# Kernel tuning notes

Measured on AMD Instinct MI355X. Metric: run time of the kernel, lower is better.

Reference implementation:

```python
import math
import jax, jax.numpy as jnp
from jax import lax
import numpy as np

L, B, S, H, N = 2, 1, 2048, 1024, 16
HN = H // N
EPS = 1e-5
SIGMA = 0.02
OUT_STD = SIGMA / math.sqrt(2.0 * L)


def gelu(x):
    # OpenAI tanh-approx gelu, matching gelu_impl
    return 0.5 * x * (1.0 + jnp.tanh(0.7978845608028654 * x * (1.0 + 0.044715 * x * x)))


def layer_norm(x, g, b):
    mu = jnp.mean(x, axis=-1, keepdims=True)
    var = jnp.mean(jnp.square(x - mu), axis=-1, keepdims=True)
    return (x - mu) / jnp.sqrt(var + EPS) * g + b


def setup_inputs() -> dict:
    key = jax.random.key(0)
    ks = jax.random.split(key, 8)
    x = jax.random.normal(ks[0], (B, S, H), dtype=jnp.float32)
    ltor_mask = jnp.tril(jnp.ones((S, S), dtype=jnp.float32))[None, None]  # [1,1,S,S]
    return {
        "hidden_states": x,
        "ltor_mask": ltor_mask,
        "ln1_g": jnp.ones((L, H), jnp.float32),
        "ln1_b": jnp.zeros((L, H), jnp.float32),
        "qkv_w": jax.random.normal(ks[1], (L, H, 3 * H), jnp.float32) * SIGMA,
        "qkv_b": jnp.zeros((L, 3 * H), jnp.float32),
        "dense_w": jax.random.normal(ks[2], (L, H, H), jnp.float32) * OUT_STD,
        "dense_b": jnp.zeros((L, H), jnp.float32),
        "ln2_g": jnp.ones((L, H), jnp.float32),
        "ln2_b": jnp.zeros((L, H), jnp.float32),
        "fc_w": jax.random.normal(ks[3], (L, H, 4 * H), jnp.float32) * SIGMA,
        "fc_b": jnp.zeros((L, 4 * H), jnp.float32),
        "proj_w": jax.random.normal(ks[4], (L, 4 * H, H), jnp.float32) * OUT_STD,
        "proj_b": jnp.zeros((L, H), jnp.float32),
        "lnf_g": jnp.ones((H,), jnp.float32),
        "lnf_b": jnp.zeros((H,), jnp.float32),
    }


def _transformer(hidden_states, ltor_mask, ln1_g, ln1_b, qkv_w, qkv_b, dense_w, dense_b,
                 ln2_g, ln2_b, fc_w, fc_b, proj_w, proj_b, lnf_g, lnf_b):
    scale = 1.0 / math.sqrt(HN)

    def step(h, p):
        g1, b1, qw, qb, dw, db, g2, b2, fw, fb, pw, pb = p
        y = layer_norm(h, g1, b1)
        qkv = y @ qw + qb                       # [B,S,3H]
        q, k, v = jnp.split(qkv, 3, axis=-1)
        # [B,S,H] -> [B,N,S,HN]
        q = q.reshape(B, S, N, HN).transpose(0, 2, 1, 3)
        k = k.reshape(B, S, N, HN).transpose(0, 2, 1, 3)
        v = v.reshape(B, S, N, HN).transpose(0, 2, 1, 3)
        scores = jnp.einsum('bnqd,bnkd->bnqk', q, k) * scale
        scores = scores * ltor_mask - 10000.0 * (1.0 - ltor_mask)
        probs = jax.nn.softmax(scores, axis=-1)
        ctx = jnp.einsum('bnqk,bnkd->bnqd', probs, v)
        ctx = ctx.transpose(0, 2, 1, 3).reshape(B, S, H)
        attn_out = ctx @ dw + db
        h2 = h + attn_out
        y2 = layer_norm(h2, g2, b2)
        mlp_out = gelu(y2 @ fw + fb) @ pw + pb
        return h2 + mlp_out, None

    params = (ln1_g, ln1_b, qkv_w, qkv_b, dense_w, dense_b,
              ln2_g, ln2_b, fc_w, fc_b, proj_w, proj_b)
    h, _ = lax.scan(step, hidden_states, params)
    return layer_norm(h, lnf_g, lnf_b)


def reference(hidden_states, ltor_mask, ln1_g, ln1_b, qkv_w, qkv_b, dense_w, dense_b,
              ln2_g, ln2_b, fc_w, fc_b, proj_w, proj_b, lnf_g, lnf_b):
    return _transformer(hidden_states, ltor_mask, ln1_g, ln1_b, qkv_w, qkv_b,
                        dense_w, dense_b, ln2_g, ln2_b, fc_w, fc_b,
                        proj_w, proj_b, lnf_g, lnf_b)
```

## Files before the change

kernel.cpp:

```cpp
#include <hip/hip_runtime.h>
#include <hip/hip_bf16.h>
#include <cstdint>
#include <cstddef>

typedef __bf16 bf16;
typedef __attribute__((ext_vector_type(4))) __bf16 bf16x4;
typedef __attribute__((ext_vector_type(8))) __bf16 bf16x8;
typedef __attribute__((ext_vector_type(4))) float floatx4;

__global__ __launch_bounds__(256) void ln_first(const float* __restrict__ x,
                                                float* __restrict__ h,
                                                const float* __restrict__ g,
                                                const float* __restrict__ b,
                                                bf16* __restrict__ y) {
    __shared__ float red[8];
    const int row = blockIdx.x, tid = threadIdx.x;
    const size_t off = (size_t)row * 1024 + tid * 4;
    const float4 v = *(const float4*)(x + off);
    *(float4*)(h + off) = v;
    float s = v.x + v.y + v.z + v.w;
#pragma unroll
    for (int o = 32; o > 0; o >>= 1) s += __shfl_xor(s, o);
    if ((tid & 63) == 0) red[tid >> 6] = s;
    __syncthreads();
    const float mean = (red[0] + red[1] + red[2] + red[3]) * (1.f / 1024.f);
    const float d[4] = {v.x - mean, v.y - mean, v.z - mean, v.w - mean};
    float q = d[0] * d[0] + d[1] * d[1] + d[2] * d[2] + d[3] * d[3];
#pragma unroll
    for (int o = 32; o > 0; o >>= 1) q += __shfl_xor(q, o);
    if ((tid & 63) == 0) red[4 + (tid >> 6)] = q;
    __syncthreads();
    const float var = (red[4] + red[5] + red[6] + red[7]) * (1.f / 1024.f);
    const float rstd = rsqrtf(var + 1e-5f);
    const int base = tid * 4;
#pragma unroll
    for (int i = 0; i < 4; i++)
        y[off + i] = (bf16)(d[i] * rstd * g[base + i] + b[base + i]);
}

template <typename OutT, int KS>
__global__ __launch_bounds__(256) void reduce_ln(const bf16* __restrict__ part,
                                                 const float* __restrict__ bias,
                                                 float* __restrict__ h,
                                                 const float* __restrict__ g,
                                                 const float* __restrict__ b,
                                                 OutT* __restrict__ y) {
    __shared__ float red[8];
    const int row = blockIdx.x, tid = threadIdx.x;
    const int base = tid * 4;
    const size_t off = (size_t)row * 1024 + base;
    const float4 hv = *(const float4*)(h + off);
    const float4 bv = *(const float4*)(bias + base);
    float a[4] = {hv.x + bv.x, hv.y + bv.y, hv.z + bv.z, hv.w + bv.w};
#pragma unroll
    for (int z = 0; z < KS; z++) {
        bf16x4 pv = *(const bf16x4*)(part + (size_t)z * (2048 * 1024) + off);
#pragma unroll
        for (int i = 0; i < 4; i++) a[i] += (float)pv[i];
    }
    *(float4*)(h + off) = (float4){a[0], a[1], a[2], a[3]};
    float s = a[0] + a[1] + a[2] + a[3];
#pragma unroll
    for (int o = 32; o > 0; o >>= 1) s += __shfl_xor(s, o);
    if ((tid & 63) == 0) red[tid >> 6] = s;
    __syncthreads();
    const float mean = (red[0] + red[1] + red[2] + red[3]) * (1.f / 1024.f);
    const float d[4] = {a[0] - mean, a[1] - mean, a[2] - mean, a[3] - mean};
    float q = d[0] * d[0] + d[1] * d[1] + d[2] * d[2] + d[3] * d[3];
#pragma unroll
    for (int o = 32; o > 0; o >>= 1) q += __shfl_xor(q, o);
    if ((tid & 63) == 0) red[4 + (tid >> 6)] = q;
    __syncthreads();
    const float var = (red[4] + red[5] + red[6] + red[7]) * (1.f / 1024.f);
    const float rstd = rsqrtf(var + 1e-5f);
#pragma unroll
    for (int i = 0; i < 4; i++)
        y[off + i] = (OutT)(d[i] * rstd * g[base + i] + b[base + i]);
}

__global__ __launch_bounds__(256) void transpose_cvt(const float* __restrict__ in,
                                                     bf16* __restrict__ out, int K, int N) {
    __shared__ float T[64][65];
    const int k0 = blockIdx.x * 64, n0 = blockIdx.y * 64;
    {
        const int r = threadIdx.x >> 4;
        const int c4 = (threadIdx.x & 15) * 4;
#pragma unroll
        for (int j = 0; j < 4; j++) {
            float4 v = *(const float4*)&in[(size_t)(k0 + r + j * 16) * N + n0 + c4];
            T[r + j * 16][c4 + 0] = v.x; T[r + j * 16][c4 + 1] = v.y;
            T[r + j * 16][c4 + 2] = v.z; T[r + j * 16][c4 + 3] = v.w;
        }
    }
    __syncthreads();
    {
        const int rn = threadIdx.x >> 3;
        const int c8 = (threadIdx.x & 7) * 8;
#pragma unroll
        for (int j = 0; j < 2; j++) {
            bf16x8 v;
#pragma unroll
            for (int i = 0; i < 8; i++) v[i] = (bf16)T[c8 + i][rn + j * 32];
            *(bf16x8*)&out[(size_t)(n0 + rn + j * 32) * K + k0 + c8] = v;
        }
    }
}

template <int MODE, int BM>
__global__ __launch_bounds__(256) void gemm_bt(const bf16* __restrict__ A,
                                               const bf16* __restrict__ BT,
                                               const float* __restrict__ bias,
                                               bf16* __restrict__ outb,
                                               int M, int N, int K) {
    constexpr int MS = BM / 32;
    constexpr int AC = BM / 32;
    constexpr int LS = 72;
    __shared__ bf16 As[BM * LS];
    __shared__ bf16 Bs[128 * LS];
    const int tid = threadIdx.x;
    const int w = tid >> 6, lane = tid & 63;
    const int quad = lane >> 4, l16 = lane & 15;
    const int wm = w >> 1, wn = w & 1;
    const int m0 = blockIdx.x * BM, n0 = blockIdx.y * 128;
    const int kchunk = K / gridDim.z;
    const int kbeg = blockIdx.z * kchunk, kend = kbeg + kchunk;

    const int srow = lane >> 3;
    const int scol = (lane & 7) * 8;
    const int arow = w * (BM / 4) + srow;
    const int brow = w * 32 + srow;
    const bf16* ga = A + (size_t)(m0 + arow) * K + scol;
    const bf16* gb = BT + (size_t)(n0 + brow) * K + scol;
    bf16* wa = &As[arow * LS + scol];
    bf16* wb = &Bs[brow * LS + scol];

    bf16x8 areg[AC], breg[4];
#pragma unroll
    for (int s = 0; s < AC; s++) areg[s] = *(const bf16x8*)(ga + (size_t)(s * 8) * K + kbeg);
#pragma unroll
    for (int s = 0; s < 4; s++) breg[s] = *(const bf16x8*)(gb + (size_t)(s * 8) * K + kbeg);

    floatx4 acc[MS][4];
#pragma unroll
    for (int i = 0; i < MS; i++)
#pragma unroll
        for (int j = 0; j < 4; j++) acc[i][j] = (floatx4){0.f, 0.f, 0.f, 0.f};

    for (int k0 = kbeg; k0 < kend; k0 += 64) {
        __syncthreads();
#pragma unroll
        for (int s = 0; s < AC; s++) *(bf16x8*)(wa + s * 8 * LS) = areg[s];
#pragma unroll
        for (int s = 0; s < 4; s++) *(bf16x8*)(wb + s * 8 * LS) = breg[s];
        __syncthreads();
        if (k0 + 64 < kend) {
#pragma unroll
            for (int s = 0; s < AC; s++) areg[s] = *(const bf16x8*)(ga + (size_t)(s * 8) * K + k0 + 64);
#pragma unroll
            for (int s = 0; s < 4; s++) breg[s] = *(const bf16x8*)(gb + (size_t)(s * 8) * K + k0 + 64);
        }
#pragma unroll
        for (int ks = 0; ks < 2; ks++) {
            bf16x8 af[MS], bfr[4];
#pragma unroll
            for (int ms = 0; ms < MS; ms++)
                af[ms] = *(const bf16x8*)&As[(wm * (BM / 2) + ms * 16 + l16) * LS + ks * 32 + quad * 8];
#pragma unroll
            for (int ns = 0; ns < 4; ns++)
                bfr[ns] = *(const bf16x8*)&Bs[(wn * 64 + ns * 16 + l16) * LS + ks * 32 + quad * 8];
#pragma unroll
            for (int ms = 0; ms < MS; ms++)
#pragma unroll
                for (int ns = 0; ns < 4; ns++)
                    acc[ms][ns] = __builtin_amdgcn_mfma_f32_16x16x32_bf16(af[ms], bfr[ns],
                                                                          acc[ms][ns], 0, 0, 0);
        }
    }

    bf16* pout = (MODE == 2) ? (outb + (size_t)blockIdx.z * M * N) : outb;
#pragma unroll
    for (int ms = 0; ms < MS; ms++) {
#pragma unroll
        for (int ns = 0; ns < 4; ns++) {
            const int row = m0 + wm * (BM / 2) + ms * 16 + quad * 4;
            const int col = n0 + wn * 64 + ns * 16 + l16;
            const float bv = (MODE == 2) ? 0.f : bias[col];
#pragma unroll
            for (int i = 0; i < 4; i++) {
                float v = acc[ms][ns][i] + bv;
                size_t idx = (size_t)(row + i) * N + col;
                if (MODE == 1) {
                    float t = 0.7978845608028654f * v * (1.f + 0.044715f * v * v);
                    pout[idx] = (bf16)(0.5f * v * (1.f + tanhf(t)));
                } else {
                    pout[idx] = (bf16)v;
                }
            }
        }
    }
}

__global__ __launch_bounds__(256) void attn_mfma(const bf16* __restrict__ qkv,
                                                 bf16* __restrict__ ctx) {
    __shared__ bf16 Ks[64][68];
    __shared__ bf16 Vt[64][72];
    __shared__ bf16 QPa[64][68];
    __shared__ bf16 QPb[64][68];
    const int tid = threadIdx.x;
    const int w = tid >> 6, lane = tid & 63;
    const int quad = lane >> 4, l16 = lane & 15;
    const int head = blockIdx.y;
    const int qta = blockIdx.x;
    const int qtb = 31 - qta;
    const int qa = qta * 64, qb = qtb * 64;
    const int rowg = w * 16 + quad * 4;
    const int r = tid >> 2;
    const int c = (tid & 3) * 16;
    const float SC = 0.18033688011111827f;

    {
        const bf16* pa = qkv + (size_t)(qa + r) * 3072 + head * 64 + c;
        const bf16* pb = qkv + (size_t)(qb + r) * 3072 + head * 64 + c;
        bf16x8 a0 = *(const bf16x8*)pa, a1 = *(const bf16x8*)(pa + 8);
        bf16x8 b0 = *(const bf16x8*)pb, b1 = *(const bf16x8*)(pb + 8);
        bf16x8 sa0, sa1, sb0, sb1;
#pragma unroll
        for (int i = 0; i < 8; i++) {
            sa0[i] = (bf16)((float)a0[i] * SC); sa1[i] = (bf16)((float)a1[i] * SC);
            sb0[i] = (bf16)((float)b0[i] * SC); sb1[i] = (bf16)((float)b1[i] * SC);
        }
        *(bf16x8*)&QPa[r][c] = sa0; *(bf16x8*)&QPa[r][c + 8] = sa1;
        *(bf16x8*)&QPb[r][c] = sb0; *(bf16x8*)&QPb[r][c + 8] = sb1;
    }
    const bf16x8 aqA0 = *(const bf16x8*)&QPa[w * 16 + l16][quad * 8];
    const bf16x8 aqA1 = *(const bf16x8*)&QPa[w * 16 + l16][32 + quad * 8];
    const bf16x8 aqB0 = *(const bf16x8*)&QPb[w * 16 + l16][quad * 8];
    const bf16x8 aqB1 = *(const bf16x8*)&QPb[w * 16 + l16][32 + quad * 8];

    float lsa[4] = {0.f, 0.f, 0.f, 0.f}, lsb[4] = {0.f, 0.f, 0.f, 0.f};
    floatx4 oa[4], ob[4];
#pragma unroll
    for (int d = 0; d < 4; d++) {
        oa[d] = (floatx4){0.f, 0.f, 0.f, 0.f};
        ob[d] = (floatx4){0.f, 0.f, 0.f, 0.f};
    }

    const int nt = qtb + 1;
    bf16x8 kr0, kr1, vr0, vr1;
    {
        const bf16* kp = qkv + (size_t)r * 3072 + 1024 + head * 64 + c;
        kr0 = *(const bf16x8*)kp; kr1 = *(const bf16x8*)(kp + 8);
        const bf16* vp = qkv + (size_t)lane * 3072 + 2048 + head * 64 + w * 16;
        vr0 = *(const bf16x8*)vp; vr1 = *(const bf16x8*)(vp + 8);
    }

    for (int t = 0; t < nt; t++) {
        __syncthreads();
        *(bf16x8*)&Ks[r][c] = kr0;
        *(bf16x8*)&Ks[r][c + 8] = kr1;
#pragma unroll
        for (int i = 0; i < 8; i++) {
            Vt[w * 16 + i][lane] = vr0[i];
            Vt[w * 16 + 8 + i][lane] = vr1[i];
        }
        __syncthreads();
        if (t + 1 < nt) {
            const size_t kb = (size_t)(t + 1) * 64;
            const bf16* kp = qkv + (kb + r) * 3072 + 1024 + head * 64 + c;
            kr0 = *(const bf16x8*)kp; kr1 = *(const bf16x8*)(kp + 8);
            const bf16* vp = qkv + (kb + lane) * 3072 + 2048 + head * 64 + w * 16;
            vr0 = *(const bf16x8*)vp; vr1 = *(const bf16x8*)(vp + 8);
        }
        const bool doA = (t <= qta);

        floatx4 s4b[4], s4a[4];
#pragma unroll
        for (int n = 0; n < 4; n++) s4b[n] = (floatx4){0.f, 0.f, 0.f, 0.f};
#pragma unroll
        for (int n = 0; n < 4; n++) {
            bf16x8 bk0 = *(const bf16x8*)&Ks[n * 16 + l16][quad * 8];
            bf16x8 bk1 = *(const bf16x8*)&Ks[n * 16 + l16][32 + quad * 8];
            s4b[n] = __builtin_amdgcn_mfma_f32_16x16x32_bf16(aqB0, bk0, s4b[n], 0, 0, 0);
            s4b[n] = __builtin_amdgcn_mfma_f32_16x16x32_bf16(aqB1, bk1, s4b[n], 0, 0, 0);
        }
        if (doA) {
#pragma unroll
            for (int n = 0; n < 4; n++) s4a[n] = (floatx4){0.f, 0.f, 0.f, 0.f};
#pragma unroll
            for (int n = 0; n < 4; n++) {
                bf16x8 bk0 = *(const bf16x8*)&Ks[n * 16 + l16][quad * 8];
                bf16x8 bk1 = *(const bf16x8*)&Ks[n * 16 + l16][32 + quad * 8];
                s4a[n] = __builtin_amdgcn_mfma_f32_16x16x32_bf16(aqA0, bk0, s4a[n], 0, 0, 0);
                s4a[n] = __builtin_amdgcn_mfma_f32_16x16x32_bf16(aqA1, bk1, s4a[n], 0, 0, 0);
            }
        }

        {
            float p[4][4];
            if (t == nt - 1) {
#pragma unroll
                for (int i = 0; i < 4; i++)
#pragma unroll
                    for (int n = 0; n < 4; n++)
                        p[n][i] = (n * 16 + l16 > rowg + i) ? 0.f
                                  : __builtin_amdgcn_exp2f(s4b[n][i]);
            } else {
#pragma unroll
                for (int i = 0; i < 4; i++)
#pragma unroll
                    for (int n = 0; n < 4; n++)
                        p[n][i] = __builtin_amdgcn_exp2f(s4b[n][i]);
            }
#pragma unroll
            for (int i = 0; i < 4; i++)
#pragma unroll
                for (int n = 0; n < 4; n++) lsb[i] += p[n][i];
#pragma unroll
            for (int n = 0; n < 4; n++)
#pragma unroll
                for (int i = 0; i < 4; i++)
                    QPb[rowg + i][n * 16 + l16] = (bf16)p[n][i];
        }
        if (doA) {
            float p[4][4];
            if (t == qta) {
#pragma unroll
                for (int i = 0; i < 4; i++)
#pragma unroll
                    for (int n = 0; n < 4; n++)
                        p[n][i] = (n * 16 + l16 > rowg + i) ? 0.f
                                  : __builtin_amdgcn_exp2f(s4a[n][i]);
            } else {
#pragma unroll
                for (int i = 0; i < 4; i++)
#pragma unroll
                    for (int n = 0; n < 4; n++)
                        p[n][i] = __builtin_amdgcn_exp2f(s4a[n][i]);
            }
#pragma unroll
            for (int i = 0; i < 4; i++)
#pragma unroll
                for (int n = 0; n < 4; n++) lsa[i] += p[n][i];
#pragma unroll
            for (int n = 0; n < 4; n++)
#pragma unroll
                for (int i = 0; i < 4; i++)
                    QPa[rowg + i][n * 16 + l16] = (bf16)p[n][i];
        }

        {
            bf16x8 ap0 = *(const bf16x8*)&QPb[w * 16 + l16][quad * 8];
            bf16x8 ap1 = *(const bf16x8*)&QPb[w * 16 + l16][32 + quad * 8];
#pragma unroll
            for (int d = 0; d < 4; d++) {
                bf16x8 bv0 = *(const bf16x8*)&Vt[d * 16 + l16][quad * 8];
                bf16x8 bv1 = *(const bf16x8*)&Vt[d * 16 + l16][32 + quad * 8];
                ob[d] = __builtin_amdgcn_mfma_f32_16x16x32_bf16(ap0, bv0, ob[d], 0, 0, 0);
                ob[d] = __builtin_amdgcn_mfma_f32_16x16x32_bf16(ap1, bv1, ob[d], 0, 0, 0);
            }
        }
        if (doA) {
            bf16x8 ap0 = *(const bf16x8*)&QPa[w * 16 + l16][quad * 8];
            bf16x8 ap1 = *(const bf16x8*)&QPa[w * 16 + l16][32 + quad * 8];
#pragma unroll
            for (int d = 0; d < 4; d++) {
                bf16x8 bv0 = *(const bf16x8*)&Vt[d * 16 + l16][quad * 8];
                bf16x8 bv1 = *(const bf16x8*)&Vt[d * 16 + l16][32 + quad * 8];
                oa[d] = __builtin_amdgcn_mfma_f32_16x16x32_bf16(ap0, bv0, oa[d], 0, 0, 0);
                oa[d] = __builtin_amdgcn_mfma_f32_16x16x32_bf16(ap1, bv1, oa[d], 0, 0, 0);
            }
        }
    }

#pragma unroll
    for (int i = 0; i < 4; i++) {
#pragma unroll
        for (int msk = 1; msk < 16; msk <<= 1) {
            lsb[i] += __shfl_xor(lsb[i], msk);
            lsa[i] += __shfl_xor(lsa[i], msk);
        }
    }
#pragma unroll
    for (int i = 0; i < 4; i++) {
        const float rlb = 1.f / lsb[i];
        const float rla = 1.f / lsa[i];
        const size_t rbB = (size_t)(qb + rowg + i) * 1024 + head * 64;
        const size_t rbA = (size_t)(qa + rowg + i) * 1024 + head * 64;
#pragma unroll
        for (int d = 0; d < 4; d++) {
            ctx[rbB + d * 16 + l16] = (bf16)(ob[d][i] * rlb);
            ctx[rbA + d * 16 + l16] = (bf16)(oa[d][i] * rla);
        }
    }
}

extern "C" void kernel_launch(void* const* d_in, const int* in_sizes, int n_in,
                              void* d_out, int out_size, void* d_ws, size_t ws_size,
                              hipStream_t stream) {
    const float* hidden  = (const float*)d_in[0];
    const float* ln1_g   = (const float*)d_in[2];
    const float* ln1_b   = (const float*)d_in[3];
    const float* qkv_w   = (const float*)d_in[4];
    const float* qkv_b   = (const float*)d_in[5];
    const float* dense_w = (const float*)d_in[6];
    const float* dense_b = (const float*)d_in[7];
    const float* ln2_g   = (const float*)d_in[8];
    const float* ln2_b   = (const float*)d_in[9];
    const float* fc_w    = (const float*)d_in[10];
    const float* fc_b    = (const float*)d_in[11];
    const float* proj_w  = (const float*)d_in[12];
    const float* proj_b  = (const float*)d_in[13];
    const float* lnf_g   = (const float*)d_in[14];
    const float* lnf_b   = (const float*)d_in[15];

    char* ws = (char*)d_ws;
    float* h   = (float*)(ws);
    bf16* y    = (bf16*)(ws + 8u  * 1024 * 1024);
    bf16* qkv  = (bf16*)(ws + 12u * 1024 * 1024);
    bf16* ctx  = (bf16*)(ws + 24u * 1024 * 1024);
    bf16* mlp  = (bf16*)(ws + 12u * 1024 * 1024);
    bf16* wT   = (bf16*)(ws + 28u * 1024 * 1024);
    bf16* part = (bf16*)(ws + 36u * 1024 * 1024);

    ln_first<<<2048, 256, 0, stream>>>(hidden, h, ln1_g, ln1_b, y);

    for (int l = 0; l < 2; l++) {
        transpose_cvt<<<dim3(16, 48), 256, 0, stream>>>(qkv_w + (size_t)l * 1024 * 3072, wT, 1024, 3072);
        gemm_bt<0, 64><<<dim3(32, 24, 1), 256, 0, stream>>>(y, wT, qkv_b + l * 3072, qkv, 2048, 3072, 1024);

        attn_mfma<<<dim3(16, 16), 256, 0, stream>>>(qkv, ctx);

        transpose_cvt<<<dim3(16, 16), 256, 0, stream>>>(dense_w + (size_t)l * 1024 * 1024, wT, 1024, 1024);
        gemm_bt<2, 64><<<dim3(32, 8, 4), 256, 0, stream>>>(ctx, wT, nullptr, part, 2048, 1024, 1024);
        reduce_ln<bf16, 4><<<2048, 256, 0, stream>>>(part, dense_b + l * 1024, h,
                                                     ln2_g + l * 1024, ln2_b + l * 1024, y);

        transpose_cvt<<<dim3(16, 64), 256, 0, stream>>>(fc_w + (size_t)l * 1024 * 4096, wT, 1024, 4096);
        gemm_bt<1, 64><<<dim3(32, 32, 1), 256, 0, stream>>>(y, wT, fc_b + l * 4096, mlp, 2048, 4096, 1024);

        transpose_cvt<<<dim3(64, 16), 256, 0, stream>>>(proj_w + (size_t)l * 4096 * 1024, wT, 4096, 1024);
        gemm_bt<2, 64><<<dim3(32, 8, 4), 256, 0, stream>>>(mlp, wT, nullptr, part, 2048, 1024, 4096);
        if (l == 0) {
            reduce_ln<bf16, 4><<<2048, 256, 0, stream>>>(part, proj_b, h,
                                                         ln1_g + 1024, ln1_b + 1024, y);
        } else {
            reduce_ln<float, 4><<<2048, 256, 0, stream>>>(part, proj_b + 1024, h,
                                                          lnf_g, lnf_b, (float*)d_out);
        }
    }
}
```

Baseline: 472.9 us.

## Use 128x128 GEMM tiles with direct global-to-LDS loads

Replaces the BMx128 GEMM with a 128x128-tile kernel that moves global data straight into LDS via global_load_lds, skipping the register staging. Each k-step first reads all A/B fragments into registers, then issues the next tile's loads while the MFMAs run on a single LDS buffer. The larger tile raises data reuse per block and halves the grid. In exchange it drops the LDS row padding, which can cause bank conflicts on the fragment reads, and it relies on correct wait handling for the asynchronous LDS loads.

After: 469.1 us. Within noise of the previous version (-0.8%).

```diff
diff --git a/kernel.cpp b/kernel.cpp
--- a/kernel.cpp
+++ b/kernel.cpp
@@ -7,6 +7,12 @@
 typedef __attribute__((ext_vector_type(4))) __bf16 bf16x4;
 typedef __attribute__((ext_vector_type(8))) __bf16 bf16x8;
 typedef __attribute__((ext_vector_type(4))) float floatx4;
+
+__device__ __forceinline__ void gload16(const bf16* g, bf16* l) {
+    __builtin_amdgcn_global_load_lds(
+        (const __attribute__((address_space(1))) void*)g,
+        (__attribute__((address_space(3))) void*)l, 16, 0, 0);
+}
 
 __global__ __launch_bounds__(256) void ln_first(const float* __restrict__ x,
                                                 float* __restrict__ h,
@@ -106,83 +112,76 @@
     }
 }
 
-template <int MODE, int BM>
-__global__ __launch_bounds__(256) void gemm_bt(const bf16* __restrict__ A,
-                                               const bf16* __restrict__ BT,
-                                               const float* __restrict__ bias,
-                                               bf16* __restrict__ outb,
-                                               int M, int N, int K) {
-    constexpr int MS = BM / 32;
-    constexpr int AC = BM / 32;
-    constexpr int LS = 72;
-    __shared__ bf16 As[BM * LS];
-    __shared__ bf16 Bs[128 * LS];
+template <int MODE>
+__global__ __launch_bounds__(256) void gemm_bt128(const bf16* __restrict__ A,
+                                                  const bf16* __restrict__ BT,
+                                                  const float* __restrict__ bias,
+                                                  bf16* __restrict__ outb,
+                                                  int M, int N, int K) {
+    __shared__ bf16 As[128 * 64];
+    __shared__ bf16 Bs[128 * 64];
     const int tid = threadIdx.x;
     const int w = tid >> 6, lane = tid & 63;
     const int quad = lane >> 4, l16 = lane & 15;
     const int wm = w >> 1, wn = w & 1;
-    const int m0 = blockIdx.x * BM, n0 = blockIdx.y * 128;
+    const int m0 = blockIdx.x * 128, n0 = blockIdx.y * 128;
     const int kchunk = K / gridDim.z;
-    const int kbeg = blockIdx.z * kchunk, kend = kbeg + kchunk;
+    const int kbeg = blockIdx.z * kchunk;
 
     const int srow = lane >> 3;
     const int scol = (lane & 7) * 8;
-    const int arow = w * (BM / 4) + srow;
-    const int brow = w * 32 + srow;
-    const bf16* ga = A + (size_t)(m0 + arow) * K + scol;
-    const bf16* gb = BT + (size_t)(n0 + brow) * K + scol;
-    bf16* wa = &As[arow * LS + scol];
-    bf16* wb = &Bs[brow * LS + scol];
-
-    bf16x8 areg[AC], breg[4];
-#pragma unroll
-    for (int s = 0; s < AC; s++) areg[s] = *(const bf16x8*)(ga + (size_t)(s * 8) * K + kbeg);
-#pragma unroll
-    for (int s = 0; s < 4; s++) breg[s] = *(const bf16x8*)(gb + (size_t)(s * 8) * K + kbeg);
-
-    floatx4 acc[MS][4];
-#pragma unroll
-    for (int i = 0; i < MS; i++)
+    const bf16* ga = A + (size_t)(m0 + w * 32 + srow) * K + kbeg + scol;
+    const bf16* gb = BT + (size_t)(n0 + w * 32 + srow) * K + kbeg + scol;
+    bf16* la = As + (w * 32) * 64;
+    bf16* lb = Bs + (w * 32) * 64;
+
+    floatx4 acc[4][4];
+#pragma unroll
+    for (int i = 0; i < 4; i++)
 #pragma unroll
         for (int j = 0; j < 4; j++) acc[i][j] = (floatx4){0.f, 0.f, 0.f, 0.f};
 
-    for (int k0 = kbeg; k0 < kend; k0 += 64) {
+#pragma unroll
+    for (int s = 0; s < 4; s++) {
+        gload16(ga + (size_t)(s * 8) * K, la + s * 8 * 64);
+        gload16(gb + (size_t)(s * 8) * K, lb + s * 8 * 64);
+    }
+
+    for (int kk = 0; kk < kchunk; kk += 64) {
         __syncthreads();
-#pragma unroll
-        for (int s = 0; s < AC; s++) *(bf16x8*)(wa + s * 8 * LS) = areg[s];
-#pragma unroll
-        for (int s = 0; s < 4; s++) *(bf16x8*)(wb + s * 8 * LS) = breg[s];
+        bf16x8 af[2][4], bfr[2][4];
+#pragma unroll
+        for (int ks = 0; ks < 2; ks++) {
+#pragma unroll
+            for (int i = 0; i < 4; i++) {
+                af[ks][i]  = *(const bf16x8*)&As[(wm * 64 + i * 16 + l16) * 64 + ks * 32 + quad * 8];
+                bfr[ks][i] = *(const bf16x8*)&Bs[(wn * 64 + i * 16 + l16) * 64 + ks * 32 + quad * 8];
+            }
+        }
         __syncthreads();
-        if (k0 + 64 < kend) {
-#pragma unroll
-            for (int s = 0; s < AC; s++) areg[s] = *(const bf16x8*)(ga + (size_t)(s * 8) * K + k0 + 64);
-#pragma unroll
-            for (int s = 0; s < 4; s++) breg[s] = *(const bf16x8*)(gb + (size_t)(s * 8) * K + k0 + 64);
-        }
-#pragma unroll
-        for (int ks = 0; ks < 2; ks++) {
-            bf16x8 af[MS], bfr[4];
-#pragma unroll
-            for (int ms = 0; ms < MS; ms++)
-                af[ms] = *(const bf16x8*)&As[(wm * (BM / 2) + ms * 16 + l16) * LS + ks * 32 + quad * 8];
-#pragma unroll
-            for (int ns = 0; ns < 4; ns++)
-                bfr[ns] = *(const bf16x8*)&Bs[(wn * 64 + ns * 16 + l16) * LS + ks * 32 + quad * 8];
-#pragma unroll
-            for (int ms = 0; ms < MS; ms++)
+        if (kk + 64 < kchunk) {
+#pragma unroll
+            for (int s = 0; s < 4; s++) {
+                gload16(ga + (size_t)(s * 8) * K + kk + 64, la + s * 8 * 64);
+                gload16(gb + (size_t)(s * 8) * K + kk + 64, lb + s * 8 * 64);
+            }
+        }
+#pragma unroll
+        for (int ks = 0; ks < 2; ks++)
+#pragma unroll
+            for (int ms = 0; ms < 4; ms++)
 #pragma unroll
                 for (int ns = 0; ns < 4; ns++)
-                    acc[ms][ns] = __builtin_amdgcn_mfma_f32_16x16x32_bf16(af[ms], bfr[ns],
+                    acc[ms][ns] = __builtin_amdgcn_mfma_f32_16x16x32_bf16(af[ks][ms], bfr[ks][ns],
                                                                           acc[ms][ns], 0, 0, 0);
-        }
     }
 
     bf16* pout = (MODE == 2) ? (outb + (size_t)blockIdx.z * M * N) : outb;
 #pragma unroll
-    for (int ms = 0; ms < MS; ms++) {
+    for (int ms = 0; ms < 4; ms++) {
 #pragma unroll
         for (int ns = 0; ns < 4; ns++) {
-            const int row = m0 + wm * (BM / 2) + ms * 16 + quad * 4;
+            const int row = m0 + wm * 64 + ms * 16 + quad * 4;
             const int col = n0 + wn * 64 + ns * 16 + l16;
             const float bv = (MODE == 2) ? 0.f : bias[col];
 #pragma unroll
@@ -426,20 +425,20 @@
 
     for (int l = 0; l < 2; l++) {
         transpose_cvt<<<dim3(16, 48), 256, 0, stream>>>(qkv_w + (size_t)l * 1024 * 3072, wT, 1024, 3072);
-        gemm_bt<0, 64><<<dim3(32, 24, 1), 256, 0, stream>>>(y, wT, qkv_b + l * 3072, qkv, 2048, 3072, 1024);
+        gemm_bt128<0><<<dim3(16, 24, 1), 256, 0, stream>>>(y, wT, qkv_b + l * 3072, qkv, 2048, 3072, 1024);
 
         attn_mfma<<<dim3(16, 16), 256, 0, stream>>>(qkv, ctx);
 
         transpose_cvt<<<dim3(16, 16), 256, 0, stream>>>(dense_w + (size_t)l * 1024 * 1024, wT, 1024, 1024);
-        gemm_bt<2, 64><<<dim3(32, 8, 4), 256, 0, stream>>>(ctx, wT, nullptr, part, 2048, 1024, 1024);
+        gemm_bt128<2><<<dim3(16, 8, 4), 256, 0, stream>>>(ctx, wT, nullptr, part, 2048, 1024, 1024);
         reduce_ln<bf16, 4><<<2048, 256, 0, stream>>>(part, dense_b + l * 1024, h,
                                                      ln2_g + l * 1024, ln2_b + l * 1024, y);
 
         transpose_cvt<<<dim3(16, 64), 256, 0, stream>>>(fc_w + (size_t)l * 1024 * 4096, wT, 1024, 4096);
-        gemm_bt<1, 64><<<dim3(32, 32, 1), 256, 0, stream>>>(y, wT, fc_b + l * 4096, mlp, 2048, 4096, 1024);
+        gemm_bt128<1><<<dim3(16, 32, 1), 256, 0, stream>>>(y, wT, fc_b + l * 4096, mlp, 2048, 4096, 1024);
 
         transpose_cvt<<<dim3(64, 16), 256, 0, stream>>>(proj_w + (size_t)l * 4096 * 1024, wT, 4096, 1024);
-        gemm_bt<2, 64><<<dim3(32, 8, 4), 256, 0, stream>>>(mlp, wT, nullptr, part, 2048, 1024, 4096);
+        gemm_bt128<2><<<dim3(16, 8, 4), 256, 0, stream>>>(mlp, wT, nullptr, part, 2048, 1024, 4096);
         if (l == 0) {
             reduce_ln<bf16, 4><<<2048, 256, 0, stream>>>(part, proj_b, h,
                                                          ln1_g + 1024, ln1_b + 1024, y);
```
